# Performance work log

Measured on AMD Instinct MI355X. Metric: run time of the kernel, lower is better.

Reference implementation:

```python
import jax, jax.numpy as jnp
import numpy as np

N = 100_000   # atoms
B = 10_000    # building blocks
E = 320_000   # edges (bb <- atom)
D = 256       # embed_dim
H = 8         # heads
HD = D // H   # head_dim = 32
DIST = 64     # gaussian dist embed dim
MAX_R = 10.0


def setup_inputs() -> dict:
    key = jax.random.key(0)
    ks = jax.random.split(key, 10)
    atom_feats = jax.random.normal(ks[0], (N, D), jnp.float32)
    coords = jax.random.normal(ks[1], (N, 3), jnp.float32) * 3.0
    bb_vec = jnp.sort(jax.random.randint(ks[2], (N,), 0, B, jnp.int32))
    src = jax.random.randint(ks[3], (E,), 0, N, jnp.int32)
    tgt = jax.random.randint(ks[4], (E,), 0, B, jnp.int32)
    # linear params, [in, out] layout (x @ W + b)
    Wq = jax.random.normal(ks[5], (D, D), jnp.float32) / np.sqrt(D)
    Wk = jax.random.normal(ks[6], (D + DIST, D), jnp.float32) / np.sqrt(D + DIST)
    Wv = jax.random.normal(ks[7], (D + DIST, D), jnp.float32) / np.sqrt(D + DIST)
    Wo = jax.random.normal(ks[8], (D, D), jnp.float32) / np.sqrt(D)
    bq = jnp.zeros((D,), jnp.float32)
    bk = jnp.zeros((D,), jnp.float32)
    bv = jnp.zeros((D,), jnp.float32)
    bo = jnp.zeros((D,), jnp.float32)
    return dict(atom_feats=atom_feats, coords=coords, Wq=Wq, bq=bq, Wk=Wk, bk=bk,
                Wv=Wv, bv=bv, Wo=Wo, bo=bo, bb_vec=bb_vec, src=src, tgt=tgt)


def _gaussian_smearing(dist):
    offsets = jnp.linspace(0.0, MAX_R, DIST)            # [DIST]
    coeff = -0.5 / (offsets[1] - offsets[0]) ** 2
    return jnp.exp(coeff * (dist[:, None] - offsets) ** 2)  # [E, DIST]


def reference(atom_feats, coords, Wq, bq, Wk, bk, Wv, bv, Wo, bo, bb_vec, src, tgt):
    # building-block centers: mean coords, summed feats per bb
    counts = jax.ops.segment_sum(jnp.ones((N,), coords.dtype), bb_vec, num_segments=B)
    bb_center_pos = jax.ops.segment_sum(coords, bb_vec, num_segments=B)
    bb_center_pos = bb_center_pos / jnp.maximum(counts, 1.0)[:, None]       # [B, 3]
    bb_center_feats = jax.ops.segment_sum(atom_feats, bb_vec, num_segments=B)  # [B, D]

    # per-edge distance embedding
    edge_vec = coords[src] - bb_center_pos[tgt]                             # [E, 3]
    dist = jnp.sqrt(jnp.sum(edge_vec * edge_vec, axis=-1))                  # [E]
    edge_dist_embed = _gaussian_smearing(dist)                              # [E, DIST]

    # QKV
    q = (bb_center_feats @ Wq + bq).reshape(B, H, HD)                       # [B, H, HD]
    atom_input = jnp.concatenate([atom_feats[src], edge_dist_embed], -1)    # [E, D+DIST]
    k = (atom_input @ Wk + bk).reshape(E, H, HD)
    v = (atom_input @ Wv + bv).reshape(E, H, HD)

    # per-edge attention logits + segment softmax over tgt
    attn = jnp.einsum('ehc,ehc->eh', q[tgt], k) / np.sqrt(HD)               # [E, H]
    seg_max = jax.ops.segment_max(attn, tgt, num_segments=B)                # [B, H]
    ex = jnp.exp(attn - seg_max[tgt])
    denom = jax.ops.segment_sum(ex, tgt, num_segments=B)                    # [B, H]
    attn = ex / (denom[tgt] + 1e-16)

    # weighted scatter-sum of messages
    msg = attn[..., None] * v                                               # [E, H, HD]
    out = jax.ops.segment_sum(msg, tgt, num_segments=B).reshape(B, D)       # [B, D]
    return out @ Wo + bo
```

## Files before the change

kernel.cpp:

```cpp
#include <hip/hip_runtime.h>
#include <math.h>

#define N_ATOMS 100000
#define B_BB    10000
#define E_EDGES 320000
#define D_DIM   256
#define NHEAD   8
#define NDIST   64
#define EPAD    128

#define DELTA   (10.0f/63.0f)
#define GCOEFF  (-0.5f/(DELTA*DELTA))
#define QKSCALE 0.17677669529663687f

__global__ void k_offsets(const int* __restrict__ bb_vec, int* __restrict__ atom_off,
                          int* __restrict__ edge_cnt) {
  int b = blockIdx.x * 256 + threadIdx.x;
  if (b <= B_BB) {
    int lo = 0, hi = N_ATOMS;
    while (lo < hi) { int mid = (lo + hi) >> 1; if (bb_vec[mid] < b) lo = mid + 1; else hi = mid; }
    atom_off[b] = lo;
  }
  if (b < B_BB) edge_cnt[b] = 0;
}

__global__ __launch_bounds__(256) void k_bb_centers(
    const float* __restrict__ af, const float* __restrict__ coords,
    const int* __restrict__ atom_off, float* __restrict__ bbF, float* __restrict__ bb_pos) {
  int t = threadIdx.x;
  for (int b = blockIdx.x; b < B_BB; b += gridDim.x) {
    int s = atom_off[b], e = atom_off[b + 1];
    float acc = 0.f;
    for (int a = s; a < e; a++) acc += af[(size_t)a * D_DIM + t];
    bbF[(size_t)b * D_DIM + t] = acc;
    if (t < 3) {
      float c = 0.f;
      for (int a = s; a < e; a++) c += coords[(size_t)a * 3 + t];
      float cnt = (float)(e - s);
      bb_pos[b * 4 + t] = c / fmaxf(cnt, 1.0f);
    }
  }
}

__global__ __launch_bounds__(256) void k_gemm256(
    const float* __restrict__ A, const float* __restrict__ W,
    const float* __restrict__ bias, float* __restrict__ C, int M) {
  __shared__ __align__(16) float As[32][132];
  __shared__ __align__(16) float Ws[32][68];
  int tid = threadIdx.x;
  int tx = tid & 15, ty = tid >> 4;
  int row0 = blockIdx.x * 128, col0 = blockIdx.y * 64;
  float acc[8][4] = {};
  for (int k0 = 0; k0 < 256; k0 += 32) {
    {
      int r = tid >> 1, c0 = (tid & 1) * 16;
      int row = row0 + r;
      const float* ap = A + (size_t)row * 256 + k0 + c0;
#pragma unroll
      for (int jj = 0; jj < 4; ++jj) {
        float4 v = make_float4(0.f, 0.f, 0.f, 0.f);
        if (row < M) v = *(const float4*)(ap + 4 * jj);
        As[c0 + 4*jj + 0][r] = v.x; As[c0 + 4*jj + 1][r] = v.y;
        As[c0 + 4*jj + 2][r] = v.z; As[c0 + 4*jj + 3][r] = v.w;
      }
    }
    {
      int r = tid >> 3, c0 = (tid & 7) * 8;
      const float* wp = W + (size_t)(k0 + r) * 256 + col0 + c0;
      float4 v0 = *(const float4*)(wp);
      float4 v1 = *(const float4*)(wp + 4);
      *(float4*)&Ws[r][c0] = v0;
      *(float4*)&Ws[r][c0 + 4] = v1;
    }
    __syncthreads();
#pragma unroll
    for (int kk = 0; kk < 32; ++kk) {
      float4 a0 = *(const float4*)&As[kk][ty * 8];
      float4 a1 = *(const float4*)&As[kk][ty * 8 + 4];
      float4 b4 = *(const float4*)&Ws[kk][tx * 4];
      float av[8] = {a0.x, a0.y, a0.z, a0.w, a1.x, a1.y, a1.z, a1.w};
      float bv4[4] = {b4.x, b4.y, b4.z, b4.w};
#pragma unroll
      for (int i = 0; i < 8; ++i)
#pragma unroll
        for (int j = 0; j < 4; ++j) acc[i][j] += av[i] * bv4[j];
    }
    __syncthreads();
  }
#pragma unroll
  for (int i = 0; i < 8; ++i) {
    int row = row0 + ty * 8 + i;
    if (row < M) {
      int col = col0 + tx * 4;
      float4 r = make_float4(acc[i][0] + bias[col + 0], acc[i][1] + bias[col + 1],
                             acc[i][2] + bias[col + 2], acc[i][3] + bias[col + 3]);
      *(float4*)&C[(size_t)row * 256 + col] = r;
    }
  }
}

__global__ void k_hist(const int* __restrict__ tgt, int* __restrict__ edge_cnt) {
  int e = blockIdx.x * 256 + threadIdx.x;
  if (e < E_EDGES) atomicAdd(&edge_cnt[tgt[e]], 1);
}

__global__ __launch_bounds__(1024) void k_scan(
    const int* __restrict__ edge_cnt, int* __restrict__ edge_start, int* __restrict__ cursor,
    int* __restrict__ src_sorted, float* __restrict__ dist_sorted) {
  __shared__ int ssum[1024];
  int tid = threadIdx.x;
  int base = tid * 10;
  int v[10]; int s = 0;
#pragma unroll
  for (int k = 0; k < 10; k++) { int i = base + k; v[k] = (i < B_BB) ? edge_cnt[i] : 0; s += v[k]; }
  ssum[tid] = s;
  __syncthreads();
  for (int off = 1; off < 1024; off <<= 1) {
    int t = (tid >= off) ? ssum[tid - off] : 0;
    __syncthreads();
    ssum[tid] += t;
    __syncthreads();
  }
  int excl = ssum[tid] - s;
#pragma unroll
  for (int k = 0; k < 10; k++) {
    int i = base + k;
    if (i < B_BB) { edge_start[i] = excl; cursor[i] = excl; }
    excl += v[k];
  }
  if (tid == 1023) edge_start[B_BB] = E_EDGES;
  if (tid < EPAD) { src_sorted[E_EDGES + tid] = 0; dist_sorted[E_EDGES + tid] = 0.f; }
}

__global__ void k_fill(const int* __restrict__ src, const int* __restrict__ tgt,
                       const float* __restrict__ coords, const float* __restrict__ bb_pos,
                       int* __restrict__ cursor, int* __restrict__ src_sorted,
                       float* __restrict__ dist_sorted) {
  int e = blockIdx.x * 256 + threadIdx.x;
  if (e >= E_EDGES) return;
  int b = tgt[e], a = src[e];
  int pos = atomicAdd(&cursor[b], 1);
  float dx = coords[a * 3 + 0] - bb_pos[b * 4 + 0];
  float dy = coords[a * 3 + 1] - bb_pos[b * 4 + 1];
  float dz = coords[a * 3 + 2] - bb_pos[b * 4 + 2];
  src_sorted[pos] = a;
  dist_sorted[pos] = sqrtf(dx * dx + dy * dy + dz * dz);
}

__global__ __launch_bounds__(256) void k_wt(
    const float* __restrict__ q, const float* __restrict__ Wk, float* __restrict__ wt) {
  __shared__ __align__(16) float As[32][132];
  __shared__ __align__(16) float Bs[32][68];
  int tid = threadIdx.x;
  int b0 = blockIdx.x * 128;
  int i0 = blockIdx.y * 64;
  int h  = blockIdx.z;
  {
    int r = tid >> 1, c0 = (tid & 1) * 16;
    int row = b0 + r;
    const float* qp = q + (size_t)row * 256 + h * 32 + c0;
#pragma unroll
    for (int jj = 0; jj < 4; ++jj) {
      float4 v = make_float4(0.f, 0.f, 0.f, 0.f);
      if (row < B_BB) v = *(const float4*)(qp + 4 * jj);
      As[c0 + 4*jj + 0][r] = v.x; As[c0 + 4*jj + 1][r] = v.y;
      As[c0 + 4*jj + 2][r] = v.z; As[c0 + 4*jj + 3][r] = v.w;
    }
  }
  {
    int r = tid >> 2, c0 = (tid & 3) * 8;
    const float* wp = Wk + (size_t)(i0 + r) * 256 + h * 32 + c0;
#pragma unroll
    for (int jj = 0; jj < 2; ++jj) {
      float4 v = *(const float4*)(wp + 4 * jj);
      Bs[c0 + 4*jj + 0][r] = v.x; Bs[c0 + 4*jj + 1][r] = v.y;
      Bs[c0 + 4*jj + 2][r] = v.z; Bs[c0 + 4*jj + 3][r] = v.w;
    }
  }
  __syncthreads();
  int tx = tid & 15, ty = tid >> 4;
  float acc[8][4] = {};
#pragma unroll
  for (int kk = 0; kk < 32; ++kk) {
    float4 a0 = *(const float4*)&As[kk][ty * 8];
    float4 a1 = *(const float4*)&As[kk][ty * 8 + 4];
    float4 b4 = *(const float4*)&Bs[kk][tx * 4];
    float av[8] = {a0.x, a0.y, a0.z, a0.w, a1.x, a1.y, a1.z, a1.w};
    float bv4[4] = {b4.x, b4.y, b4.z, b4.w};
#pragma unroll
    for (int i = 0; i < 8; ++i)
#pragma unroll
      for (int j = 0; j < 4; ++j) acc[i][j] += av[i] * bv4[j];
  }
#pragma unroll
  for (int i = 0; i < 8; ++i) {
    int row = b0 + ty * 8 + i;
    if (row < B_BB) {
      float4 o = make_float4(acc[i][0] * QKSCALE, acc[i][1] * QKSCALE,
                             acc[i][2] * QKSCALE, acc[i][3] * QKSCALE);
      *(float4*)&wt[(size_t)row * 2560 + h * 320 + i0 + tx * 4] = o;
    }
  }
}

#define FMA4(p, v, Wb, k) \
  p = fmaf((v).x, Wb[(k)], p);   p = fmaf((v).y, Wb[(k)+1], p); \
  p = fmaf((v).z, Wb[(k)+2], p); p = fmaf((v).w, Wb[(k)+3], p);

#define ACC4(Sarr, k, ww, v) \
  Sarr[(k)]   = fmaf(ww, (v).x, Sarr[(k)]);   Sarr[(k)+1] = fmaf(ww, (v).y, Sarr[(k)+1]); \
  Sarr[(k)+2] = fmaf(ww, (v).z, Sarr[(k)+2]); Sarr[(k)+3] = fmaf(ww, (v).w, Sarr[(k)+3]);

__global__ __launch_bounds__(256) void k_attn(
    const float* __restrict__ af, float* __restrict__ wtS,
    const int* __restrict__ edge_start, const int* __restrict__ src_sorted,
    const float* __restrict__ dist_sorted, float* __restrict__ wsum) {
  int tid = threadIdx.x;
  int lane = tid & 63;
  int wv = tid >> 6;
  int h0 = 2 * wv, h1 = 2 * wv + 1;
  int g = lane >> 4;
  int sub = lane & 15;
  int b = blockIdx.x;

  int s0 = edge_start[b], e1 = edge_start[b + 1];
  float* wtb = wtS + (size_t)b * 2560;
  const float* wr0 = wtb + h0 * 320;
  const float* wr1 = wtb + h1 * 320;

  float W0[16], W1[16], wd0[4], wd1[4];
#pragma unroll
  for (int j = 0; j < 4; ++j) {
    float4 t0 = *(const float4*)(wr0 + sub * 16 + 4 * j);
    float4 t1 = *(const float4*)(wr1 + sub * 16 + 4 * j);
    W0[4*j+0] = t0.x; W0[4*j+1] = t0.y; W0[4*j+2] = t0.z; W0[4*j+3] = t0.w;
    W1[4*j+0] = t1.x; W1[4*j+1] = t1.y; W1[4*j+2] = t1.z; W1[4*j+3] = t1.w;
  }
#pragma unroll
  for (int j = 0; j < 4; ++j) { wd0[j] = wr0[256 + sub + 16*j]; wd1[j] = wr1[256 + sub + 16*j]; }

  float cj[4];
#pragma unroll
  for (int j = 0; j < 4; ++j) cj[j] = (float)(sub + 16 * j) * DELTA;

  float l0 = 0.f, l1 = 0.f;
  float S0r[16] = {}, S1r[16] = {};
  float sd0[4] = {}, sd1[4] = {};

  if (s0 < e1) {
    int ia0 = src_sorted[s0 + g];
    int ia1 = src_sorted[s0 + 4 + g];
    int ia2 = src_sorted[s0 + 8 + g];
    float dd0 = dist_sorted[s0 + g];
    float dd1 = dist_sorted[s0 + 4 + g];
    float dd2 = dist_sorted[s0 + 8 + g];
    const float4* r0p = (const float4*)(af + (size_t)ia0 * 256 + sub * 16);
    const float4* r1p = (const float4*)(af + (size_t)ia1 * 256 + sub * 16);
    float4 A0 = r0p[0], A1 = r0p[1], A2 = r0p[2], A3 = r0p[3];
    float4 B0 = r1p[0], B1 = r1p[1], B2 = r1p[2], B3 = r1p[3];

    for (int eb = s0; eb < e1; eb += 4) {
      const float4* r2p = (const float4*)(af + (size_t)ia2 * 256 + sub * 16);
      float4 C0 = r2p[0], C1 = r2p[1], C2 = r2p[2], C3 = r2p[3];
      int ia3 = src_sorted[eb + 12 + g];
      float dd3 = dist_sorted[eb + 12 + g];

      float emb[4];
#pragma unroll
      for (int j = 0; j < 4; ++j) {
        float dd = dd0 - cj[j];
        emb[j] = __expf(GCOEFF * dd * dd);
      }
      float p0 = 0.f, p1 = 0.f;
      FMA4(p0, A0, W0, 0);  FMA4(p1, A0, W1, 0);
      FMA4(p0, A1, W0, 4);  FMA4(p1, A1, W1, 4);
      FMA4(p0, A2, W0, 8);  FMA4(p1, A2, W1, 8);
      FMA4(p0, A3, W0, 12); FMA4(p1, A3, W1, 12);
#pragma unroll
      for (int j = 0; j < 4; ++j) { p0 = fmaf(emb[j], wd0[j], p0); p1 = fmaf(emb[j], wd1[j], p1); }
#pragma unroll
      for (int off = 8; off > 0; off >>= 1) {
        p0 += __shfl_xor(p0, off);
        p1 += __shfl_xor(p1, off);
      }
      float w0 = __expf(p0), w1 = __expf(p1);
      if (eb + g >= e1) { w0 = 0.f; w1 = 0.f; }
      l0 += w0; l1 += w1;
      ACC4(S0r, 0,  w0, A0); ACC4(S1r, 0,  w1, A0);
      ACC4(S0r, 4,  w0, A1); ACC4(S1r, 4,  w1, A1);
      ACC4(S0r, 8,  w0, A2); ACC4(S1r, 8,  w1, A2);
      ACC4(S0r, 12, w0, A3); ACC4(S1r, 12, w1, A3);
#pragma unroll
      for (int j = 0; j < 4; ++j) {
        sd0[j] = fmaf(w0, emb[j], sd0[j]);
        sd1[j] = fmaf(w1, emb[j], sd1[j]);
      }

      A0 = B0; A1 = B1; A2 = B2; A3 = B3;
      B0 = C0; B1 = C1; B2 = C2; B3 = C3;
      dd0 = dd1; dd1 = dd2; dd2 = dd3;
      ia2 = ia3;
    }
  }

#pragma unroll
  for (int off = 16; off <= 32; off <<= 1) {
    l0 += __shfl_xor(l0, off);
    l1 += __shfl_xor(l1, off);
#pragma unroll
    for (int c = 0; c < 16; ++c) {
      S0r[c] += __shfl_xor(S0r[c], off);
      S1r[c] += __shfl_xor(S1r[c], off);
    }
#pragma unroll
    for (int j = 0; j < 4; ++j) {
      sd0[j] += __shfl_xor(sd0[j], off);
      sd1[j] += __shfl_xor(sd1[j], off);
    }
  }

  float inv0 = 1.0f / (l0 + 1e-16f), inv1 = 1.0f / (l1 + 1e-16f);
  if (g == 0) {
#pragma unroll
    for (int j = 0; j < 4; ++j) {
      float4 o0 = make_float4(S0r[4*j+0]*inv0, S0r[4*j+1]*inv0, S0r[4*j+2]*inv0, S0r[4*j+3]*inv0);
      float4 o1 = make_float4(S1r[4*j+0]*inv1, S1r[4*j+1]*inv1, S1r[4*j+2]*inv1, S1r[4*j+3]*inv1);
      *(float4*)(wtb + h0 * 320 + sub * 16 + 4 * j) = o0;
      *(float4*)(wtb + h1 * 320 + sub * 16 + 4 * j) = o1;
    }
#pragma unroll
    for (int j = 0; j < 4; ++j) {
      wtb[h0 * 320 + 256 + sub + 16 * j] = sd0[j] * inv0;
      wtb[h1 * 320 + 256 + sub + 16 * j] = sd1[j] * inv1;
    }
    if (sub == 0) {
      wsum[b * 8 + h0] = l0 * inv0;
      wsum[b * 8 + h1] = l1 * inv1;
    }
  }
}

__global__ __launch_bounds__(256) void k_out_head(
    const float* __restrict__ Sf, const float* __restrict__ Wv,
    const float* __restrict__ bv, const float* __restrict__ wsum,
    float* __restrict__ out_pre) {
  __shared__ __align__(16) float As[32][132];
  __shared__ __align__(16) float Bs[32][36];
  int tid = threadIdx.x;
  int b0 = blockIdx.x * 128;
  int h  = blockIdx.y;
  int tx = tid & 7, ty = tid >> 3;
  float acc[4][4] = {};
  for (int k0 = 0; k0 < 320; k0 += 32) {
    {
      int r = tid >> 1, c0 = (tid & 1) * 16;
      int row = b0 + r;
      const float* sp = Sf + (size_t)row * 2560 + h * 320 + k0 + c0;
#pragma unroll
      for (int jj = 0; jj < 4; ++jj) {
        float4 v = make_float4(0.f, 0.f, 0.f, 0.f);
        if (row < B_BB) v = *(const float4*)(sp + 4 * jj);
        As[c0 + 4*jj + 0][r] = v.x; As[c0 + 4*jj + 1][r] = v.y;
        As[c0 + 4*jj + 2][r] = v.z; As[c0 + 4*jj + 3][r] = v.w;
      }
    }
    {
      int r = tid >> 3, c0 = (tid & 7) * 4;
      float4 v = *(const float4*)&Wv[(size_t)(k0 + r) * 256 + h * 32 + c0];
      *(float4*)&Bs[r][c0] = v;
    }
    __syncthreads();
#pragma unroll
    for (int kk = 0; kk < 32; ++kk) {
      float4 a4 = *(const float4*)&As[kk][ty * 4];
      float4 b4 = *(const float4*)&Bs[kk][tx * 4];
      float av[4] = {a4.x, a4.y, a4.z, a4.w};
      float bv4[4] = {b4.x, b4.y, b4.z, b4.w};
#pragma unroll
      for (int i = 0; i < 4; ++i)
#pragma unroll
        for (int j = 0; j < 4; ++j) acc[i][j] += av[i] * bv4[j];
    }
    __syncthreads();
  }
  float bvv[4];
#pragma unroll
  for (int j = 0; j < 4; ++j) bvv[j] = bv[h * 32 + tx * 4 + j];
#pragma unroll
  for (int i = 0; i < 4; ++i) {
    int row = b0 + ty * 4 + i;
    if (row < B_BB) {
      float ws = wsum[row * 8 + h];
      float4 o = make_float4(acc[i][0] + ws * bvv[0], acc[i][1] + ws * bvv[1],
                             acc[i][2] + ws * bvv[2], acc[i][3] + ws * bvv[3]);
      *(float4*)&out_pre[(size_t)row * 256 + h * 32 + tx * 4] = o;
    }
  }
}

extern "C" void kernel_launch(void* const* d_in, const int* in_sizes, int n_in,
                              void* d_out, int out_size, void* d_ws, size_t ws_size,
                              hipStream_t stream) {
  const float* af     = (const float*)d_in[0];
  const float* coords = (const float*)d_in[1];
  const float* Wq     = (const float*)d_in[2];
  const float* bq     = (const float*)d_in[3];
  const float* Wk     = (const float*)d_in[4];
  const float* bk     = (const float*)d_in[5];  (void)bk;
  const float* Wv     = (const float*)d_in[6];
  const float* bv     = (const float*)d_in[7];
  const float* Wo     = (const float*)d_in[8];
  const float* bo     = (const float*)d_in[9];
  const int* bb_vec   = (const int*)d_in[10];
  const int* src      = (const int*)d_in[11];
  const int* tgt      = (const int*)d_in[12];
  float* out = (float*)d_out;
  (void)in_sizes; (void)n_in; (void)out_size; (void)ws_size;

  char* ws = (char*)d_ws;
  size_t o = 0;
  auto alloc = [&](size_t bytes) { size_t r = o; o += (bytes + 255) & ~(size_t)255; return r; };
  int*   atom_off    = (int*)(ws + alloc((B_BB + 1) * 4));
  int*   edge_cnt    = (int*)(ws + alloc((size_t)B_BB * 4));
  int*   edge_start  = (int*)(ws + alloc((B_BB + 1) * 4));
  int*   cursor      = (int*)(ws + alloc((size_t)B_BB * 4));
  int*   src_sorted  = (int*)(ws + alloc((size_t)(E_EDGES + EPAD) * 4));
  float* dist_sorted = (float*)(ws + alloc((size_t)(E_EDGES + EPAD) * 4));
  float* bbF         = (float*)(ws + alloc((size_t)B_BB * 256 * 4));
  float* bb_pos      = (float*)(ws + alloc((size_t)B_BB * 4 * 4));
  float* q           = (float*)(ws + alloc((size_t)B_BB * 256 * 4));
  float* wtS         = (float*)(ws + alloc((size_t)B_BB * 2560 * 4));
  float* wsum        = (float*)(ws + alloc((size_t)B_BB * 8 * 4));
  float* out_pre     = (float*)(ws + alloc((size_t)B_BB * 256 * 4));

  k_offsets<<<(B_BB + 1 + 255) / 256, 256, 0, stream>>>(bb_vec, atom_off, edge_cnt);
  k_bb_centers<<<2560, 256, 0, stream>>>(af, coords, atom_off, bbF, bb_pos);
  k_hist<<<(E_EDGES + 255) / 256, 256, 0, stream>>>(tgt, edge_cnt);
  k_scan<<<1, 1024, 0, stream>>>(edge_cnt, edge_start, cursor, src_sorted, dist_sorted);
  k_fill<<<(E_EDGES + 255) / 256, 256, 0, stream>>>(src, tgt, coords, bb_pos, cursor,
                                                    src_sorted, dist_sorted);
  k_gemm256<<<dim3((B_BB + 127) / 128, 4), 256, 0, stream>>>(bbF, Wq, bq, q, B_BB);
  k_wt<<<dim3((B_BB + 127) / 128, 5, 8), 256, 0, stream>>>(q, Wk, wtS);
  k_attn<<<B_BB, 256, 0, stream>>>(af, wtS, edge_start, src_sorted, dist_sorted, wsum);
  k_out_head<<<dim3((B_BB + 127) / 128, 8), 256, 0, stream>>>(wtS, Wv, bv, wsum, out_pre);
  k_gemm256<<<dim3((B_BB + 127) / 128, 4), 256, 0, stream>>>(out_pre, Wo, bo, out, B_BB);
}
```

Baseline: 567.3 us.

## Fuse q·Wk projection into attention kernel and shrink GEMM tiles

Removes the separate k_wt kernel and computes each building block's per-head q·Wk row on the fly inside k_attn, storing it in LDS instead of round-tripping a B×2560 buffer through global memory. The generic 256-wide GEMM is retiled from 128×64 to 64×64 output blocks with a K-step of 16, doubling the block count to improve occupancy. The fused version recomputes from Wk (320×256, likely cache-resident) per block and adds 10 KB of LDS per block, which may reduce attention occupancy. k_out_head still reads wtS, which k_attn appears to populate in code not shown here.

```diff
diff --git a/kernel.cpp b/kernel.cpp
--- a/kernel.cpp
+++ b/kernel.cpp
@@ -45,51 +45,44 @@
 __global__ __launch_bounds__(256) void k_gemm256(
     const float* __restrict__ A, const float* __restrict__ W,
     const float* __restrict__ bias, float* __restrict__ C, int M) {
-  __shared__ __align__(16) float As[32][132];
-  __shared__ __align__(16) float Ws[32][68];
+  __shared__ __align__(16) float As[16][68];
+  __shared__ __align__(16) float Ws[16][64];
   int tid = threadIdx.x;
   int tx = tid & 15, ty = tid >> 4;
-  int row0 = blockIdx.x * 128, col0 = blockIdx.y * 64;
-  float acc[8][4] = {};
-  for (int k0 = 0; k0 < 256; k0 += 32) {
+  int row0 = blockIdx.x * 64, col0 = blockIdx.y * 64;
+  float acc[4][4] = {};
+  for (int k0 = 0; k0 < 256; k0 += 16) {
     {
-      int r = tid >> 1, c0 = (tid & 1) * 16;
+      int r = tid >> 2;
+      int c = (tid & 3) * 4;
       int row = row0 + r;
-      const float* ap = A + (size_t)row * 256 + k0 + c0;
-#pragma unroll
-      for (int jj = 0; jj < 4; ++jj) {
-        float4 v = make_float4(0.f, 0.f, 0.f, 0.f);
-        if (row < M) v = *(const float4*)(ap + 4 * jj);
-        As[c0 + 4*jj + 0][r] = v.x; As[c0 + 4*jj + 1][r] = v.y;
-        As[c0 + 4*jj + 2][r] = v.z; As[c0 + 4*jj + 3][r] = v.w;
-      }
+      float4 v = make_float4(0.f, 0.f, 0.f, 0.f);
+      if (row < M) v = *(const float4*)&A[(size_t)row * 256 + k0 + c];
+      As[c + 0][r] = v.x; As[c + 1][r] = v.y; As[c + 2][r] = v.z; As[c + 3][r] = v.w;
     }
     {
-      int r = tid >> 3, c0 = (tid & 7) * 8;
-      const float* wp = W + (size_t)(k0 + r) * 256 + col0 + c0;
-      float4 v0 = *(const float4*)(wp);
-      float4 v1 = *(const float4*)(wp + 4);
-      *(float4*)&Ws[r][c0] = v0;
-      *(float4*)&Ws[r][c0 + 4] = v1;
-    }
-    __syncthreads();
-#pragma unroll
-    for (int kk = 0; kk < 32; ++kk) {
-      float4 a0 = *(const float4*)&As[kk][ty * 8];
-      float4 a1 = *(const float4*)&As[kk][ty * 8 + 4];
-      float4 b4 = *(const float4*)&Ws[kk][tx * 4];
-      float av[8] = {a0.x, a0.y, a0.z, a0.w, a1.x, a1.y, a1.z, a1.w};
-      float bv4[4] = {b4.x, b4.y, b4.z, b4.w};
-#pragma unroll
-      for (int i = 0; i < 8; ++i)
-#pragma unroll
-        for (int j = 0; j < 4; ++j) acc[i][j] += av[i] * bv4[j];
-    }
-    __syncthreads();
-  }
-#pragma unroll
-  for (int i = 0; i < 8; ++i) {
-    int row = row0 + ty * 8 + i;
+      int r = tid >> 4;
+      int c = (tid & 15) * 4;
+      float4 v = *(const float4*)&W[(size_t)(k0 + r) * 256 + col0 + c];
+      *(float4*)&Ws[r][c] = v;
+    }
+    __syncthreads();
+#pragma unroll
+    for (int kk = 0; kk < 16; kk++) {
+      float4 a = *(const float4*)&As[kk][ty * 4];
+      float4 b = *(const float4*)&Ws[kk][tx * 4];
+      float av[4] = {a.x, a.y, a.z, a.w};
+      float bv4[4] = {b.x, b.y, b.z, b.w};
+#pragma unroll
+      for (int i = 0; i < 4; i++)
+#pragma unroll
+        for (int j = 0; j < 4; j++) acc[i][j] += av[i] * bv4[j];
+    }
+    __syncthreads();
+  }
+#pragma unroll
+  for (int i = 0; i < 4; i++) {
+    int row = row0 + ty * 4 + i;
     if (row < M) {
       int col = col0 + tx * 4;
       float4 r = make_float4(acc[i][0] + bias[col + 0], acc[i][1] + bias[col + 1],
@@ -147,62 +140,6 @@
   dist_sorted[pos] = sqrtf(dx * dx + dy * dy + dz * dz);
 }
 
-__global__ __launch_bounds__(256) void k_wt(
-    const float* __restrict__ q, const float* __restrict__ Wk, float* __restrict__ wt) {
-  __shared__ __align__(16) float As[32][132];
-  __shared__ __align__(16) float Bs[32][68];
-  int tid = threadIdx.x;
-  int b0 = blockIdx.x * 128;
-  int i0 = blockIdx.y * 64;
-  int h  = blockIdx.z;
-  {
-    int r = tid >> 1, c0 = (tid & 1) * 16;
-    int row = b0 + r;
-    const float* qp = q + (size_t)row * 256 + h * 32 + c0;
-#pragma unroll
-    for (int jj = 0; jj < 4; ++jj) {
-      float4 v = make_float4(0.f, 0.f, 0.f, 0.f);
-      if (row < B_BB) v = *(const float4*)(qp + 4 * jj);
-      As[c0 + 4*jj + 0][r] = v.x; As[c0 + 4*jj + 1][r] = v.y;
-      As[c0 + 4*jj + 2][r] = v.z; As[c0 + 4*jj + 3][r] = v.w;
-    }
-  }
-  {
-    int r = tid >> 2, c0 = (tid & 3) * 8;
-    const float* wp = Wk + (size_t)(i0 + r) * 256 + h * 32 + c0;
-#pragma unroll
-    for (int jj = 0; jj < 2; ++jj) {
-      float4 v = *(const float4*)(wp + 4 * jj);
-      Bs[c0 + 4*jj + 0][r] = v.x; Bs[c0 + 4*jj + 1][r] = v.y;
-      Bs[c0 + 4*jj + 2][r] = v.z; Bs[c0 + 4*jj + 3][r] = v.w;
-    }
-  }
-  __syncthreads();
-  int tx = tid & 15, ty = tid >> 4;
-  float acc[8][4] = {};
-#pragma unroll
-  for (int kk = 0; kk < 32; ++kk) {
-    float4 a0 = *(const float4*)&As[kk][ty * 8];
-    float4 a1 = *(const float4*)&As[kk][ty * 8 + 4];
-    float4 b4 = *(const float4*)&Bs[kk][tx * 4];
-    float av[8] = {a0.x, a0.y, a0.z, a0.w, a1.x, a1.y, a1.z, a1.w};
-    float bv4[4] = {b4.x, b4.y, b4.z, b4.w};
-#pragma unroll
-    for (int i = 0; i < 8; ++i)
-#pragma unroll
-      for (int j = 0; j < 4; ++j) acc[i][j] += av[i] * bv4[j];
-  }
-#pragma unroll
-  for (int i = 0; i < 8; ++i) {
-    int row = b0 + ty * 8 + i;
-    if (row < B_BB) {
-      float4 o = make_float4(acc[i][0] * QKSCALE, acc[i][1] * QKSCALE,
-                             acc[i][2] * QKSCALE, acc[i][3] * QKSCALE);
-      *(float4*)&wt[(size_t)row * 2560 + h * 320 + i0 + tx * 4] = o;
-    }
-  }
-}
-
 #define FMA4(p, v, Wb, k) \
   p = fmaf((v).x, Wb[(k)], p);   p = fmaf((v).y, Wb[(k)+1], p); \
   p = fmaf((v).z, Wb[(k)+2], p); p = fmaf((v).w, Wb[(k)+3], p);
@@ -212,9 +149,11 @@
   Sarr[(k)+2] = fmaf(ww, (v).z, Sarr[(k)+2]); Sarr[(k)+3] = fmaf(ww, (v).w, Sarr[(k)+3]);
 
 __global__ __launch_bounds__(256) void k_attn(
-    const float* __restrict__ af, float* __restrict__ wtS,
+    const float* __restrict__ af, const float* __restrict__ q,
+    const float* __restrict__ Wk, float* __restrict__ wtS,
     const int* __restrict__ edge_start, const int* __restrict__ src_sorted,
     const float* __restrict__ dist_sorted, float* __restrict__ wsum) {
+  __shared__ __align__(16) float wt_lds[NHEAD * 320];
   int tid = threadIdx.x;
   int lane = tid & 63;
   int wv = tid >> 6;
@@ -224,9 +163,32 @@
   int b = blockIdx.x;
 
   int s0 = edge_start[b], e1 = edge_start[b + 1];
+
+  {
+    int h = tid >> 5, il = tid & 31;
+    const float* qh = q + (size_t)b * 256 + h * 32;
+    float4 qv[8];
+#pragma unroll
+    for (int j = 0; j < 8; ++j) qv[j] = *(const float4*)(qh + 4 * j);
+#pragma unroll
+    for (int k = 0; k < 10; ++k) {
+      int i = il + 32 * k;
+      const float* wkp = Wk + (size_t)i * 256 + h * 32;
+      float p = 0.f;
+#pragma unroll
+      for (int j = 0; j < 8; ++j) {
+        float4 wk4 = *(const float4*)(wkp + 4 * j);
+        p = fmaf(qv[j].x, wk4.x, p); p = fmaf(qv[j].y, wk4.y, p);
+        p = fmaf(qv[j].z, wk4.z, p); p = fmaf(qv[j].w, wk4.w, p);
+      }
+      wt_lds[h * 320 + i] = p * QKSCALE;
+    }
+  }
+  __syncthreads();
+
   float* wtb = wtS + (size_t)b * 2560;
-  const float* wr0 = wtb + h0 * 320;
-  const float* wr1 = wtb + h1 * 320;
+  const float* wr0 = wt_lds + h0 * 320;
+  const float* wr1 = wt_lds + h1 * 320;
 
   float W0[16], W1[16], wd0[4], wd1[4];
 #pragma unroll
@@ -439,9 +401,8 @@
   k_scan<<<1, 1024, 0, stream>>>(edge_cnt, edge_start, cursor, src_sorted, dist_sorted);
   k_fill<<<(E_EDGES + 255) / 256, 256, 0, stream>>>(src, tgt, coords, bb_pos, cursor,
                                                     src_sorted, dist_sorted);
-  k_gemm256<<<dim3((B_BB + 127) / 128, 4), 256, 0, stream>>>(bbF, Wq, bq, q, B_BB);
-  k_wt<<<dim3((B_BB + 127) / 128, 5, 8), 256, 0, stream>>>(q, Wk, wtS);
-  k_attn<<<B_BB, 256, 0, stream>>>(af, wtS, edge_start, src_sorted, dist_sorted, wsum);
+  k_gemm256<<<dim3((B_BB + 63) / 64, 4), 256, 0, stream>>>(bbF, Wq, bq, q, B_BB);
+  k_attn<<<B_BB, 256, 0, stream>>>(af, q, Wk, wtS, edge_start, src_sorted, dist_sorted, wsum);
   k_out_head<<<dim3((B_BB + 127) / 128, 8), 256, 0, stream>>>(wtS, Wv, bv, wsum, out_pre);
-  k_gemm256<<<dim3((B_BB + 127) / 128, 4), 256, 0, stream>>>(out_pre, Wo, bo, out, B_BB);
-}
+  k_gemm256<<<dim3((B_BB + 63) / 64, 4), 256, 0, stream>>>(out_pre, Wo, bo, out, B_BB);
+}
```

Measured after the change: 1.051 ms. 85.3% more time.
